# Optimization experiments

Measured on AMD Instinct MI355X. Metric: run time of the kernel, lower is better.

## Reference

```python
import jax, jax.numpy as jnp
import numpy as np

N = 50000
DIM_IN = 256
HID = 64
OUT = 32
E1 = 800000
E2 = 1600000
BN_EPS = 1e-5


def _make_edges(rng, n, e):
    row = rng.integers(0, n, size=e).astype(np.int32)
    col = rng.integers(0, n, size=e).astype(np.int32)
    # gcn_norm without self loops: val = d^{-1/2}[row] * d^{-1/2}[col]
    deg = np.bincount(row, minlength=n) + 0.0
    deg_c = np.bincount(col, minlength=n) + 0.0
    dr = 1.0 / np.sqrt(np.maximum(deg, 1.0))
    dc = 1.0 / np.sqrt(np.maximum(deg_c, 1.0))
    val = (dr[row] * dc[col]).astype(np.float32)
    return row, col, val


def setup_inputs() -> dict:
    key = jax.random.key(0)
    ks = jax.random.split(key, 4)
    rng = np.random.default_rng(0)
    e1_row, e1_col, e1_val = _make_edges(rng, N, E1)
    e2_row, e2_col, e2_val = _make_edges(rng, N, E2)
    return {
        "x": jax.random.normal(ks[0], (N, DIM_IN), dtype=jnp.float32),
        "e1_row": jnp.asarray(e1_row), "e1_col": jnp.asarray(e1_col), "e1_val": jnp.asarray(e1_val),
        "e2_row": jnp.asarray(e2_row), "e2_col": jnp.asarray(e2_col), "e2_val": jnp.asarray(e2_val),
        "W_embed": jax.random.normal(ks[1], (DIM_IN, HID), dtype=jnp.float32) * (1.0 / np.sqrt(DIM_IN)),
        "b_embed": jnp.zeros((HID,), dtype=jnp.float32),
        "bn0_gamma": jnp.ones((2 * HID,), dtype=jnp.float32),
        "bn0_beta": jnp.zeros((2 * HID,), dtype=jnp.float32),
        "bn1_gamma": jnp.ones((4 * HID,), dtype=jnp.float32),
        "bn1_beta": jnp.zeros((4 * HID,), dtype=jnp.float32),
        "W_head": jax.random.normal(ks[2], (15 * HID, OUT), dtype=jnp.float32) * (1.0 / np.sqrt(15 * HID)),
        "b_head": jnp.zeros((OUT,), dtype=jnp.float32),
    }


def _spmm(row, col, val, x, n):
    # out[row] += val * x[col]  (sparse [n,n] @ dense [n,d])
    return jax.ops.segment_sum(val[:, None] * x[col], row, num_segments=n)


def _bn(v, gamma, beta):
    # BatchNorm1d training-mode math: per-feature mean / biased var over nodes
    m = jnp.mean(v, axis=0)
    var = jnp.mean(jnp.square(v - m), axis=0)
    return gamma * (v - m) * jax.lax.rsqrt(var + BN_EPS) + beta


def reference(x, e1_row, e1_col, e1_val, e2_row, e2_col, e2_val,
              W_embed, b_embed, bn0_gamma, bn0_beta, bn1_gamma, bn1_beta,
              W_head, b_head):
    n = x.shape[0]

    def conv(h):
        h1 = _spmm(e1_row, e1_col, e1_val, h, n)
        h2 = _spmm(e2_row, e2_col, e2_val, h, n)
        return jnp.concatenate([h1, h2], axis=1)

    h = jax.nn.relu(x @ W_embed + b_embed)          # [n, HID]
    xs = [h]
    c0 = _bn(conv(h), bn0_gamma, bn0_beta)           # [n, 2*HID]
    xs.append(c0)
    c1 = _bn(conv(c0), bn1_gamma, bn1_beta)          # [n, 4*HID]
    xs.append(c1)
    c2 = conv(c1)                                    # [n, 8*HID]
    xs.append(c2)
    j = jnp.concatenate(xs, axis=1)                  # [n, 15*HID]
    return j @ W_head + b_head                       # [n, OUT]
```

## Files before the change

### kernel.cpp

```cpp
#include <hip/hip_runtime.h>


#define NN  50000
#define E1N 800000
#define E2N 1600000
#define LD  960
#define NT  3125
#define NBKT 391
#define CHUNK 2048
#define G1B 391
#define G2B 782
#define NCG 7

typedef short bf16x8 __attribute__((ext_vector_type(8)));
typedef float f32x4  __attribute__((ext_vector_type(4)));
typedef float f32x2  __attribute__((ext_vector_type(2)));

__device__ __forceinline__ float bfl(unsigned int w) { return __uint_as_float(w << 16); }
__device__ __forceinline__ float bfh(unsigned int w) { return __uint_as_float(w & 0xFFFF0000u); }
__device__ __forceinline__ float bf2f(unsigned short u) { return __uint_as_float(((unsigned int)u) << 16); }
__device__ __forceinline__ unsigned short f2bf(float f) {
    unsigned int u = __float_as_uint(f);
    u += 0x7FFFu + ((u >> 16) & 1u);
    return (unsigned short)(u >> 16);
}
__device__ __forceinline__ unsigned int pack2(float a, float b) {
    return (unsigned int)f2bf(a) | ((unsigned int)f2bf(b) << 16);
}
__device__ __forceinline__ unsigned int packfp8(float a, float b, float c, float d) {
    int w = __builtin_amdgcn_cvt_pk_fp8_f32(a, b, 0, false);
    w     = __builtin_amdgcn_cvt_pk_fp8_f32(c, d, w, true);
    return (unsigned int)w;
}
__device__ __forceinline__ f32x2 pkfma(f32x2 a, f32x2 b, f32x2 c) {
#if __has_builtin(__builtin_elementwise_fma)
    return __builtin_elementwise_fma(a, b, c);
#else
    return (f32x2){fmaf(a[0], b[0], c[0]), fmaf(a[1], b[1], c[1])};
#endif
}
__device__ __forceinline__ f32x2 bf2(unsigned int w) {
    return (f32x2){bfl(w), bfh(w)};
}


__global__ __launch_bounds__(256) void zero_kernel(float* c, int nc) {
    int i = blockIdx.x * 256 + threadIdx.x;
    if (i < nc) c[i] = 0.f;
}

__global__ __launch_bounds__(256) void bucket_count_kernel(const int* __restrict__ r1,
                                                           const int* __restrict__ r2,
                                                           int* __restrict__ bc1, int* __restrict__ bc2) {
    __shared__ int cnt[NBKT];
    for (int t = threadIdx.x; t < NBKT; t += 256) cnt[t] = 0;
    __syncthreads();
    int blk = blockIdx.x;
    const int* r; int base, lim; int* bc;
    if (blk < G1B) { r = r1; base = blk * CHUNK; lim = min(base + CHUNK, E1N); bc = bc1 + blk * NBKT; }
    else { int b2 = blk - G1B; r = r2; base = b2 * CHUNK; lim = min(base + CHUNK, E2N); bc = bc2 + b2 * NBKT; }
    for (int i = base + threadIdx.x; i < lim; i += 256)
        atomicAdd(&cnt[r[i] >> 7], 1);
    __syncthreads();
    for (int t = threadIdx.x; t < NBKT; t += 256) bc[t] = cnt[t];
}

__global__ __launch_bounds__(512) void bucket_scan_kernel(int* __restrict__ bc1, int* __restrict__ bc2) {
    __shared__ int s[512];
    int t = threadIdx.x;
    int tot1 = 0, tot2 = 0;
    if (t < NBKT) {
        for (int b = 0; b < G1B; b++) tot1 += bc1[b * NBKT + t];
        for (int b = 0; b < G2B; b++) tot2 += bc2[b * NBKT + t];
    }
    s[t] = (t < NBKT) ? tot1 : 0;
    __syncthreads();
    for (int off = 1; off < 512; off <<= 1) {
        int v = (t >= off) ? s[t - off] : 0;
        __syncthreads(); s[t] += v; __syncthreads();
    }
    int base1 = ((t < NBKT) ? s[t] : 0) - tot1;
    __syncthreads();
    s[t] = (t < NBKT) ? tot2 : 0;
    __syncthreads();
    for (int off = 1; off < 512; off <<= 1) {
        int v = (t >= off) ? s[t - off] : 0;
        __syncthreads(); s[t] += v; __syncthreads();
    }
    int base2 = ((t < NBKT) ? s[t] : 0) - tot2;
    if (t < NBKT) {
        int run = base1;
        for (int b = 0; b < G1B; b++) { int v = bc1[b * NBKT + t]; bc1[b * NBKT + t] = run; run += v; }
        run = base2;
        for (int b = 0; b < G2B; b++) { int v = bc2[b * NBKT + t]; bc2[b * NBKT + t] = run; run += v; }
    }
}

__global__ __launch_bounds__(256) void bucket_place_kernel(
        const int* __restrict__ r1, const int* __restrict__ c1, const float* __restrict__ v1,
        const int* __restrict__ r2, const int* __restrict__ c2, const float* __restrict__ v2,
        const int* __restrict__ bc1, const int* __restrict__ bc2,
        uint2* __restrict__ T1, uint2* __restrict__ T2) {
    __shared__ int pos[NBKT];
    int blk = blockIdx.x;
    const int *r, *c; const float* v; int base, lim; const int* bc; uint2* T;
    if (blk < G1B) { r = r1; c = c1; v = v1; base = blk * CHUNK; lim = min(base + CHUNK, E1N);
                     bc = bc1 + blk * NBKT; T = T1; }
    else { int b2 = blk - G1B; r = r2; c = c2; v = v2; base = b2 * CHUNK; lim = min(base + CHUNK, E2N);
           bc = bc2 + b2 * NBKT; T = T2; }
    for (int t = threadIdx.x; t < NBKT; t += 256) pos[t] = bc[t];
    __syncthreads();
    for (int i = base + threadIdx.x; i < lim; i += 256) {
        int row = r[i];
        int p = atomicAdd(&pos[row >> 7], 1);
        T[p] = make_uint2(((unsigned)c[i] << 16) | (unsigned)row, __float_as_uint(v[i]));
    }
}

__global__ __launch_bounds__(256) void bucket_sort_kernel(
        const int* __restrict__ bb1, const uint2* __restrict__ T1, int* __restrict__ rp1, unsigned int* __restrict__ Ed1,
        const int* __restrict__ bb2, const uint2* __restrict__ T2, int* __restrict__ rp2, unsigned int* __restrict__ Ed2) {
    int b = blockIdx.x % NBKT;
    int g = blockIdx.x / NBKT;
    const int* bb = g ? bb2 : bb1;
    const uint2* T = g ? T2 : T1;
    int* rp = g ? rp2 : rp1;
    unsigned int* Ed = g ? Ed2 : Ed1;
    int EN = g ? E2N : E1N;
    int beg = bb[b];
    int end = (b == NBKT - 1) ? EN : bb[b + 1];
    int R0 = b * 128;
    int nrows = min(128, NN - R0);
    __shared__ int cnt[1024];
    __shared__ int cur[896];
    __shared__ int ps[256];
    int t = threadIdx.x;
    for (int i = t; i < 1024; i += 256) cnt[i] = 0;
    __syncthreads();
    for (int i = beg + t; i < end; i += 256) {
        unsigned int x = T[i].x;
        int lr = (x & 0xFFFFu) & 127;
        int cg = (int)(x >> 29);
        atomicAdd(&cnt[lr * NCG + cg + 1], 1);
    }
    __syncthreads();
    int b0 = t * 4;
    int c0 = cnt[b0], c1 = cnt[b0 + 1], c2 = cnt[b0 + 2], c3 = cnt[b0 + 3];
    int s1 = c0 + c1, s2 = s1 + c2, s3 = s2 + c3;
    ps[t] = s3;
    __syncthreads();
    for (int off = 1; off < 256; off <<= 1) {
        int v = (t >= off) ? ps[t - off] : 0;
        __syncthreads(); ps[t] += v; __syncthreads();
    }
    int base = (t > 0) ? ps[t - 1] : 0;
    cnt[b0] = base + c0; cnt[b0 + 1] = base + s1;
    cnt[b0 + 2] = base + s2; cnt[b0 + 3] = base + s3;
    __syncthreads();
    for (int k = t; k < 896; k += 256) cur[k] = beg + cnt[k];
    if (t < nrows) rp[R0 + t] = beg + cnt[t * NCG];
    if (b == NBKT - 1 && t == 0) rp[NN] = end;
    __syncthreads();
    for (int i = beg + t; i < end; i += 256) {
        uint2 rec = T[i];
        int lr = (rec.x & 0xFFFFu) & 127;
        int cg = (int)(rec.x >> 29);
        int p = atomicAdd(&cur[lr * NCG + cg], 1);
        Ed[p] = (rec.x & 0xFFFF0000u) | (unsigned)f2bf(__uint_as_float(rec.y));
    }
}

__global__ __launch_bounds__(256) void packw_kernel(const float* __restrict__ W, unsigned short* __restrict__ Wb,
                                                    int NC, int kbs, int total) {
    int i = blockIdx.x * 256 + threadIdx.x;
    if (i >= total) return;
    int lane  = i & 63;
    int kb    = (i >> 6) % kbs;
    int ctile = i / (kbs * 64);
    int n  = ctile * 16 + (lane & 15);
    int k0 = kb * 32 + (lane >> 4) * 8;
    unsigned short v[8];
    #pragma unroll
    for (int j = 0; j < 8; j++) v[j] = f2bf(W[(k0 + j) * NC + n]);
    *(uint4*)(Wb + (size_t)i * 8) = *(uint4*)v;
}

__global__ __launch_bounds__(256) void embed_mfma_kernel(const float* __restrict__ x,
                                                         const unsigned short* __restrict__ Wb,
                                                         const float* __restrict__ bias,
                                                         unsigned short* __restrict__ Jh) {
    int wave = threadIdx.x >> 6;
    int lane = threadIdx.x & 63;
    int tile = blockIdx.x * 4 + wave;
    if (tile >= NT) return;
    int m = lane & 15;
    int q = lane >> 4;
    const float* xr = x + (size_t)(tile * 16 + m) * 256 + q * 8;
    const unsigned short* bbase = Wb + (size_t)lane * 8;
    f32x4 acc[4];
    #pragma unroll
    for (int ct = 0; ct < 4; ct++) acc[ct] = (f32x4){0.f, 0.f, 0.f, 0.f};
    #pragma unroll
    for (int kb = 0; kb < 8; kb++) {
        float4 xa = *(const float4*)(xr + kb * 32);
        float4 xb = *(const float4*)(xr + kb * 32 + 4);
        unsigned short av[8];
        av[0] = f2bf(xa.x); av[1] = f2bf(xa.y); av[2] = f2bf(xa.z); av[3] = f2bf(xa.w);
        av[4] = f2bf(xb.x); av[5] = f2bf(xb.y); av[6] = f2bf(xb.z); av[7] = f2bf(xb.w);
        bf16x8 a = *(bf16x8*)av;
        #pragma unroll
        for (int ct = 0; ct < 4; ct++) {
            bf16x8 bfr = *(const bf16x8*)(bbase + (size_t)(ct * 8 + kb) * 512);
            acc[ct] = __builtin_amdgcn_mfma_f32_16x16x32_bf16(a, bfr, acc[ct], 0, 0, 0);
        }
    }
    #pragma unroll
    for (int ct = 0; ct < 4; ct++) {
        int col = ct * 16 + m;
        float bb = bias[col];
        #pragma unroll
        for (int r = 0; r < 4; r++) {
            float v = fmaxf(acc[ct][r] + bb, 0.f);
            Jh[(size_t)(tile * 16 + q * 4 + r) * LD + col] = f2bf(v);
        }
    }
}

template <int LPR>
__global__ __launch_bounds__(256) void spmm_bf16x8_kernel(
        const int* __restrict__ rp1, const unsigned int* __restrict__ ed1,
        const int* __restrict__ rp2, const unsigned int* __restrict__ ed2,
        const unsigned short* __restrict__ src, unsigned short* __restrict__ dst) {
    constexpr int ROWS = 64 / LPR;
    constexpr int SRCF = LPR * 8;
    constexpr int RPB  = ROWS * 4;
    constexpr int GB   = (NN + RPB - 1) / RPB;
    int g    = (blockIdx.x >= GB) ? 1 : 0;
    int bx   = blockIdx.x - g * GB;
    int wave = threadIdx.x >> 6;
    int lane = threadIdx.x & 63;
    int grp  = lane / LPR;
    int sub  = lane % LPR;
    int row  = (bx * 4 + wave) * ROWS + grp;
    const int*          rp = g ? rp2 : rp1;
    const unsigned int* ed = g ? ed2 : ed1;
    bool ok = row < NN;
    int beg = 0, end = 0;
    if (ok) { beg = rp[row]; end = rp[row + 1]; }

    f32x2 acc[4];
    #pragma unroll
    for (int u = 0; u < 4; u++) acc[u] = (f32x2){0.f, 0.f};
    const unsigned short* sbase = src + sub * 8;

    int j = beg;
    for (; j + 8 <= end; j += 8) {
        unsigned int e[8];
        #pragma unroll
        for (int u = 0; u < 8; u++) e[u] = ed[j + u];
        uint4 s[8];
        #pragma unroll
        for (int u = 0; u < 8; u++) s[u] = *(const uint4*)(sbase + (size_t)(e[u] >> 16) * LD);
        #pragma unroll
        for (int u = 0; u < 8; u++) {
            float v = bfl(e[u]);
            f32x2 vv = (f32x2){v, v};
            acc[0] = pkfma(vv, bf2(s[u].x), acc[0]);
            acc[1] = pkfma(vv, bf2(s[u].y), acc[1]);
            acc[2] = pkfma(vv, bf2(s[u].z), acc[2]);
            acc[3] = pkfma(vv, bf2(s[u].w), acc[3]);
        }
    }
    for (; j < end; j++) {
        unsigned int e = ed[j];
        float v = bfl(e);
        f32x2 vv = (f32x2){v, v};
        uint4 s = *(const uint4*)(sbase + (size_t)(e >> 16) * LD);
        acc[0] = pkfma(vv, bf2(s.x), acc[0]);
        acc[1] = pkfma(vv, bf2(s.y), acc[1]);
        acc[2] = pkfma(vv, bf2(s.z), acc[2]);
        acc[3] = pkfma(vv, bf2(s.w), acc[3]);
    }

    if (ok) {
        unsigned short* dp = dst + (size_t)row * LD + g * SRCF + sub * 8;
        uint4 o;
        o.x = pack2(acc[0][0], acc[0][1]); o.y = pack2(acc[1][0], acc[1][1]);
        o.z = pack2(acc[2][0], acc[2][1]); o.w = pack2(acc[3][0], acc[3][1]);
        *(uint4*)dp = o;
    }
}

template <int LPR>
__global__ __launch_bounds__(256) void spmm_fp8x16_kernel(
        const int* __restrict__ rp1, const unsigned int* __restrict__ ed1,
        const int* __restrict__ rp2, const unsigned int* __restrict__ ed2,
        const unsigned char* __restrict__ src8,
        unsigned short* __restrict__ dst) {
    constexpr int ROWS = 64 / LPR;
    constexpr int SRCF = LPR * 16;
    constexpr int RPB  = ROWS * 4;
    constexpr int GB   = (NN + RPB - 1) / RPB;
    int g    = (blockIdx.x >= GB) ? 1 : 0;
    int bx   = blockIdx.x - g * GB;
    int wave = threadIdx.x >> 6;
    int lane = threadIdx.x & 63;
    int grp  = lane / LPR;
    int sub  = lane % LPR;
    int row  = (bx * 4 + wave) * ROWS + grp;
    const int*          rp = g ? rp2 : rp1;
    const unsigned int* ed = g ? ed2 : ed1;
    bool ok = row < NN;
    int beg = 0, end = 0;
    if (ok) { beg = rp[row]; end = rp[row + 1]; }

    f32x2 acc[8];
    #pragma unroll
    for (int u = 0; u < 8; u++) acc[u] = (f32x2){0.f, 0.f};
    const unsigned char* sbase = src8 + sub * 16;

    int j = beg;
    for (; j + 8 <= end; j += 8) {
        unsigned int e[8];
        #pragma unroll
        for (int u = 0; u < 8; u++) e[u] = ed[j + u];
        uint4 s[8];
        #pragma unroll
        for (int u = 0; u < 8; u++) s[u] = *(const uint4*)(sbase + (size_t)(e[u] >> 16) * SRCF);
        #pragma unroll
        for (int u = 0; u < 8; u++) {
            float v = bfl(e[u]);
            f32x2 vv = (f32x2){v, v};
            acc[0] = pkfma(vv, __builtin_amdgcn_cvt_pk_f32_fp8(s[u].x, false), acc[0]);
            acc[1] = pkfma(vv, __builtin_amdgcn_cvt_pk_f32_fp8(s[u].x, true),  acc[1]);
            acc[2] = pkfma(vv, __builtin_amdgcn_cvt_pk_f32_fp8(s[u].y, false), acc[2]);
            acc[3] = pkfma(vv, __builtin_amdgcn_cvt_pk_f32_fp8(s[u].y, true),  acc[3]);
            acc[4] = pkfma(vv, __builtin_amdgcn_cvt_pk_f32_fp8(s[u].z, false), acc[4]);
            acc[5] = pkfma(vv, __builtin_amdgcn_cvt_pk_f32_fp8(s[u].z, true),  acc[5]);
            acc[6] = pkfma(vv, __builtin_amdgcn_cvt_pk_f32_fp8(s[u].w, false), acc[6]);
            acc[7] = pkfma(vv, __builtin_amdgcn_cvt_pk_f32_fp8(s[u].w, true),  acc[7]);
        }
    }
    for (; j < end; j++) {
        unsigned int e = ed[j];
        float v = bfl(e);
        f32x2 vv = (f32x2){v, v};
        uint4 s = *(const uint4*)(sbase + (size_t)(e >> 16) * SRCF);
        acc[0] = pkfma(vv, __builtin_amdgcn_cvt_pk_f32_fp8(s.x, false), acc[0]);
        acc[1] = pkfma(vv, __builtin_amdgcn_cvt_pk_f32_fp8(s.x, true),  acc[1]);
        acc[2] = pkfma(vv, __builtin_amdgcn_cvt_pk_f32_fp8(s.y, false), acc[2]);
        acc[3] = pkfma(vv, __builtin_amdgcn_cvt_pk_f32_fp8(s.y, true),  acc[3]);
        acc[4] = pkfma(vv, __builtin_amdgcn_cvt_pk_f32_fp8(s.z, false), acc[4]);
        acc[5] = pkfma(vv, __builtin_amdgcn_cvt_pk_f32_fp8(s.z, true),  acc[5]);
        acc[6] = pkfma(vv, __builtin_amdgcn_cvt_pk_f32_fp8(s.w, false), acc[6]);
        acc[7] = pkfma(vv, __builtin_amdgcn_cvt_pk_f32_fp8(s.w, true),  acc[7]);
    }

    if (ok) {
        unsigned short* dp = dst + (size_t)row * LD + g * SRCF + sub * 16;
        uint4 o1, o2;
        o1.x = pack2(acc[0][0], acc[0][1]); o1.y = pack2(acc[1][0], acc[1][1]);
        o1.z = pack2(acc[2][0], acc[2][1]); o1.w = pack2(acc[3][0], acc[3][1]);
        o2.x = pack2(acc[4][0], acc[4][1]); o2.y = pack2(acc[5][0], acc[5][1]);
        o2.z = pack2(acc[6][0], acc[6][1]); o2.w = pack2(acc[7][0], acc[7][1]);
        *(uint4*)dp = o1;
        *(uint4*)(dp + 8) = o2;
    }
}

template <int F>
__global__ __launch_bounds__(256) void bn_stats_kernel(const unsigned short* __restrict__ c,
                                                       float* sum, float* sumsq) {
    constexpr int SL = 256 / F;
    int f  = threadIdx.x % F;
    int sl = threadIdx.x / F;
    float s = 0.f, ss = 0.f;
    for (int r = blockIdx.x * SL + sl; r < NN; r += gridDim.x * SL) {
        float v = bf2f(c[(size_t)r * LD + f]);
        s += v; ss += v * v;
    }
    __shared__ float ls[256], lss[256];
    ls[threadIdx.x] = s; lss[threadIdx.x] = ss;
    __syncthreads();
    if (sl == 0) {
        #pragma unroll
        for (int u = 1; u < SL; u++) { s += ls[f + u * F]; ss += lss[f + u * F]; }
        atomicAdd(&sum[f], s);
        atomicAdd(&sumsq[f], ss);
    }
}

__global__ void bn_finalize_kernel(const float* sum, const float* sumsq, const float* __restrict__ gamma,
                                   const float* __restrict__ beta, float* scale, float* shift, int F) {
    int f = blockIdx.x * blockDim.x + threadIdx.x;
    if (f >= F) return;
    float m   = sum[f] * (1.0f / NN);
    float var = sumsq[f] * (1.0f / NN) - m * m;
    float sc  = gamma[f] * rsqrtf(var + 1e-5f);
    scale[f] = sc;
    shift[f] = beta[f] - m * sc;
}

template <int F>
__global__ __launch_bounds__(256) void bn_apply_kernel(unsigned short* __restrict__ c,
                                                       const float* __restrict__ scale,
                                                       const float* __restrict__ shift) {
    constexpr int FV = F / 4;
    int idx  = blockIdx.x * 256 + threadIdx.x;
    int node = idx / FV;
    int fo   = (idx % FV) * 4;
    if (node >= NN) return;
    unsigned short* p = c + (size_t)node * LD + fo;
    uint2 v = *(uint2*)p;
    float a0 = bfl(v.x), a1 = bfh(v.x), a2 = bfl(v.y), a3 = bfh(v.y);
    float4 sc = *(const float4*)(scale + fo);
    float4 sh = *(const float4*)(shift + fo);
    a0 = fmaf(a0, sc.x, sh.x);
    a1 = fmaf(a1, sc.y, sh.y);
    a2 = fmaf(a2, sc.z, sh.z);
    a3 = fmaf(a3, sc.w, sh.w);
    v.x = pack2(a0, a1); v.y = pack2(a2, a3);
    *(uint2*)p = v;
}

__global__ __launch_bounds__(256) void bn_apply_fp8_kernel(unsigned short* __restrict__ c,
                                                           unsigned char* __restrict__ c8,
                                                           const float* __restrict__ scale,
                                                           const float* __restrict__ shift) {
    int idx  = blockIdx.x * 256 + threadIdx.x;
    int node = idx >> 6;
    int fo   = (idx & 63) * 4;
    if (node >= NN) return;
    unsigned short* p = c + (size_t)node * LD + fo;
    uint2 v = *(uint2*)p;
    float a0 = bfl(v.x), a1 = bfh(v.x), a2 = bfl(v.y), a3 = bfh(v.y);
    float4 sc = *(const float4*)(scale + fo);
    float4 sh = *(const float4*)(shift + fo);
    a0 = fmaf(a0, sc.x, sh.x);
    a1 = fmaf(a1, sc.y, sh.y);
    a2 = fmaf(a2, sc.z, sh.z);
    a3 = fmaf(a3, sc.w, sh.w);
    v.x = pack2(a0, a1); v.y = pack2(a2, a3);
    *(uint2*)p = v;
    *(unsigned int*)(c8 + (size_t)node * 256 + fo) = packfp8(a0, a1, a2, a3);
}

__global__ __launch_bounds__(256) void head_mfma_kernel(const unsigned short* __restrict__ Jh,
                                                        const unsigned short* __restrict__ Wb,
                                                        const float* __restrict__ b,
                                                        float* __restrict__ out) {
    int wave = threadIdx.x >> 6;
    int lane = threadIdx.x & 63;
    int tile = blockIdx.x * 4 + wave;
    if (tile >= NT) return;
    int m = lane & 15;
    int q = lane >> 4;
    const unsigned short* arow  = Jh + (size_t)(tile * 16 + m) * LD + q * 8;
    const unsigned short* bbase = Wb + (size_t)lane * 8;
    f32x4 acc0 = {0.f, 0.f, 0.f, 0.f};
    f32x4 acc1 = {0.f, 0.f, 0.f, 0.f};
    #pragma unroll 5
    for (int kb = 0; kb < 30; kb++) {
        bf16x8 a  = *(const bf16x8*)(arow + kb * 32);
        bf16x8 b0 = *(const bf16x8*)(bbase + (size_t)kb * 512);
        bf16x8 b1 = *(const bf16x8*)(bbase + (size_t)(30 + kb) * 512);
        acc0 = __builtin_amdgcn_mfma_f32_16x16x32_bf16(a, b0, acc0, 0, 0, 0);
        acc1 = __builtin_amdgcn_mfma_f32_16x16x32_bf16(a, b1, acc1, 0, 0, 0);
    }
    int col = m;
    float b0 = b[col], b1 = b[16 + col];
    #pragma unroll
    for (int r = 0; r < 4; r++) {
        float* op = out + (size_t)(tile * 16 + q * 4 + r) * 32 + col;
        op[0]  = acc0[r] + b0;
        op[16] = acc1[r] + b1;
    }
}


extern "C" void kernel_launch(void* const* d_in, const int* in_sizes, int n_in,
                              void* d_out, int out_size, void* d_ws, size_t ws_size,
                              hipStream_t stream) {
    const float* x      = (const float*)d_in[0];
    const int*   e1_row = (const int*)d_in[1];
    const int*   e1_col = (const int*)d_in[2];
    const float* e1_val = (const float*)d_in[3];
    const int*   e2_row = (const int*)d_in[4];
    const int*   e2_col = (const int*)d_in[5];
    const float* e2_val = (const float*)d_in[6];
    const float* W_emb  = (const float*)d_in[7];
    const float* b_emb  = (const float*)d_in[8];
    const float* bn0_g  = (const float*)d_in[9];
    const float* bn0_b  = (const float*)d_in[10];
    const float* bn1_g  = (const float*)d_in[11];
    const float* bn1_b  = (const float*)d_in[12];
    const float* W_head = (const float*)d_in[13];
    const float* b_head = (const float*)d_in[14];
    float* out = (float*)d_out;

    char* ws = (char*)d_ws;
    auto alloc = [&](size_t bytes) -> char* {
        char* p = ws;
        ws += (bytes + 255) & ~(size_t)255;
        return p;
    };
    int*   rp1   = (int*)alloc((NN + 1) * 4);
    int*   rp2   = (int*)alloc((NN + 1) * 4);
    int*   bc1   = (int*)alloc((size_t)G1B * NBKT * 4);
    int*   bc2   = (int*)alloc((size_t)G2B * NBKT * 4);
    unsigned int* Ed1 = (unsigned int*)alloc((size_t)E1N * 4);
    unsigned int* Ed2 = (unsigned int*)alloc((size_t)E2N * 4);
    float* stats = (float*)alloc(1536 * 4);
    unsigned short* Wbh  = (unsigned short*)alloc(3840 * 8 * 2);
    unsigned short* Wbe  = (unsigned short*)alloc(2048 * 8 * 2);
    unsigned char*  C1f8 = (unsigned char*)alloc((size_t)NN * 256);
    unsigned short* Jh   = (unsigned short*)alloc((size_t)NN * LD * 2);
    uint2* T1 = (uint2*)Jh;
    uint2* T2 = T1 + E1N;

    float* sum0   = stats;        float* sq0    = stats + 128;
    float* sum1   = stats + 256;  float* sq1    = stats + 512;
    float* scale0 = stats + 768;  float* shift0 = stats + 896;
    float* scale1 = stats + 1024; float* shift1 = stats + 1280;

    zero_kernel<<<3, 256, 0, stream>>>(stats, 768);
    bucket_count_kernel<<<G1B + G2B, 256, 0, stream>>>(e1_row, e2_row, bc1, bc2);
    bucket_scan_kernel<<<1, 512, 0, stream>>>(bc1, bc2);
    bucket_place_kernel<<<G1B + G2B, 256, 0, stream>>>(e1_row, e1_col, e1_val,
                                                       e2_row, e2_col, e2_val, bc1, bc2, T1, T2);
    bucket_sort_kernel<<<2 * NBKT, 256, 0, stream>>>(bc1, T1, rp1, Ed1, bc2, T2, rp2, Ed2);
    packw_kernel<<<15, 256, 0, stream>>>(W_head, Wbh, 32, 30, 3840);
    packw_kernel<<<8, 256, 0, stream>>>(W_emb, Wbe, 64, 8, 2048);

    embed_mfma_kernel<<<(NT + 3) / 4, 256, 0, stream>>>(x, Wbe, b_emb, Jh);

    spmm_bf16x8_kernel<8><<<2 * ((NN + 31) / 32), 256, 0, stream>>>(rp1, Ed1, rp2, Ed2, Jh, Jh + 64);
    bn_stats_kernel<128><<<512, 256, 0, stream>>>(Jh + 64, sum0, sq0);
    bn_finalize_kernel<<<1, 128, 0, stream>>>(sum0, sq0, bn0_g, bn0_b, scale0, shift0, 128);
    bn_apply_kernel<128><<<(NN * 32 + 255) / 256, 256, 0, stream>>>(Jh + 64, scale0, shift0);

    spmm_bf16x8_kernel<16><<<2 * (NN / 16), 256, 0, stream>>>(rp1, Ed1, rp2, Ed2, Jh + 64, Jh + 192);
    bn_stats_kernel<256><<<512, 256, 0, stream>>>(Jh + 192, sum1, sq1);
    bn_finalize_kernel<<<1, 256, 0, stream>>>(sum1, sq1, bn1_g, bn1_b, scale1, shift1, 256);
    bn_apply_fp8_kernel<<<(NN * 64 + 255) / 256, 256, 0, stream>>>(Jh + 192, C1f8, scale1, shift1);

    spmm_fp8x16_kernel<16><<<2 * (NN / 16), 256, 0, stream>>>(rp1, Ed1, rp2, Ed2, C1f8, Jh + 448);

    head_mfma_kernel<<<(NT + 3) / 4, 256, 0, stream>>>(Jh, Wbh, b_head, out);
}
```

Baseline: 632.6 us.

## Parallelize bucket offset scan across many blocks instead of single block

Replaces the single-block bucket scan, where each of 391 threads serially walked up to 782 chunk counts twice, with three kernels: a per-bucket reduction over 782 blocks, a small single-block exclusive scan of bucket totals, and a per-bucket parallel scan that writes chunk offsets. The aim is to remove a long serial, latency-bound pass from the preprocessing. It adds two extra kernel launches and a small workspace for totals and bases. scan_apply assumes at most 1024 chunks per graph, which holds for G2B=782.

```diff
diff --git a/kernel.cpp b/kernel.cpp
--- a/kernel.cpp
+++ b/kernel.cpp
@@ -65,34 +65,75 @@
     for (int t = threadIdx.x; t < NBKT; t += 256) bc[t] = cnt[t];
 }
 
-__global__ __launch_bounds__(512) void bucket_scan_kernel(int* __restrict__ bc1, int* __restrict__ bc2) {
+__global__ __launch_bounds__(256) void scan_tot_kernel(const int* __restrict__ bc1,
+                                                       const int* __restrict__ bc2,
+                                                       int* __restrict__ tot) {
+    int b = blockIdx.x % NBKT;
+    int g = blockIdx.x / NBKT;
+    const int* bc = g ? bc2 : bc1;
+    int G = g ? G2B : G1B;
+    int s = 0;
+    for (int i = threadIdx.x; i < G; i += 256) s += bc[(size_t)i * NBKT + b];
+    __shared__ int red[256];
+    red[threadIdx.x] = s;
+    __syncthreads();
+    for (int off = 128; off; off >>= 1) {
+        if ((int)threadIdx.x < off) red[threadIdx.x] += red[threadIdx.x + off];
+        __syncthreads();
+    }
+    if (threadIdx.x == 0) tot[g * NBKT + b] = red[0];
+}
+
+__global__ __launch_bounds__(512) void scan_base_kernel(const int* __restrict__ tot,
+                                                        int* __restrict__ base) {
     __shared__ int s[512];
     int t = threadIdx.x;
-    int tot1 = 0, tot2 = 0;
-    if (t < NBKT) {
-        for (int b = 0; b < G1B; b++) tot1 += bc1[b * NBKT + t];
-        for (int b = 0; b < G2B; b++) tot2 += bc2[b * NBKT + t];
-    }
-    s[t] = (t < NBKT) ? tot1 : 0;
+    int v1 = (t < NBKT) ? tot[t] : 0;
+    s[t] = v1;
     __syncthreads();
     for (int off = 1; off < 512; off <<= 1) {
         int v = (t >= off) ? s[t - off] : 0;
         __syncthreads(); s[t] += v; __syncthreads();
     }
-    int base1 = ((t < NBKT) ? s[t] : 0) - tot1;
-    __syncthreads();
-    s[t] = (t < NBKT) ? tot2 : 0;
+    if (t < NBKT) base[t] = s[t] - v1;
+    __syncthreads();
+    int v2 = (t < NBKT) ? tot[NBKT + t] : 0;
+    s[t] = v2;
     __syncthreads();
     for (int off = 1; off < 512; off <<= 1) {
         int v = (t >= off) ? s[t - off] : 0;
         __syncthreads(); s[t] += v; __syncthreads();
     }
-    int base2 = ((t < NBKT) ? s[t] : 0) - tot2;
-    if (t < NBKT) {
-        int run = base1;
-        for (int b = 0; b < G1B; b++) { int v = bc1[b * NBKT + t]; bc1[b * NBKT + t] = run; run += v; }
-        run = base2;
-        for (int b = 0; b < G2B; b++) { int v = bc2[b * NBKT + t]; bc2[b * NBKT + t] = run; run += v; }
+    if (t < NBKT) base[NBKT + t] = s[t] - v2;
+}
+
+__global__ __launch_bounds__(256) void scan_apply_kernel(int* __restrict__ bc1, int* __restrict__ bc2,
+                                                         const int* __restrict__ base) {
+    int b = blockIdx.x % NBKT;
+    int g = blockIdx.x / NBKT;
+    int* bc = g ? bc2 : bc1;
+    int G = g ? G2B : G1B;
+    int t = threadIdx.x;
+    int vals[4];
+    int loc = 0;
+    #pragma unroll
+    for (int k = 0; k < 4; k++) {
+        int idx = t * 4 + k;
+        int v = (idx < G) ? bc[(size_t)idx * NBKT + b] : 0;
+        vals[k] = v; loc += v;
+    }
+    __shared__ int s[256];
+    s[t] = loc;
+    __syncthreads();
+    for (int off = 1; off < 256; off <<= 1) {
+        int v = (t >= off) ? s[t - off] : 0;
+        __syncthreads(); s[t] += v; __syncthreads();
+    }
+    int run = base[g * NBKT + b] + ((t > 0) ? s[t - 1] : 0);
+    #pragma unroll
+    for (int k = 0; k < 4; k++) {
+        int idx = t * 4 + k;
+        if (idx < G) { int old = vals[k]; bc[(size_t)idx * NBKT + b] = run; run += old; }
     }
 }
 
@@ -508,6 +549,8 @@
     int*   rp2   = (int*)alloc((NN + 1) * 4);
     int*   bc1   = (int*)alloc((size_t)G1B * NBKT * 4);
     int*   bc2   = (int*)alloc((size_t)G2B * NBKT * 4);
+    int*   tot   = (int*)alloc(2 * NBKT * 4);
+    int*   basep = (int*)alloc(2 * NBKT * 4);
     unsigned int* Ed1 = (unsigned int*)alloc((size_t)E1N * 4);
     unsigned int* Ed2 = (unsigned int*)alloc((size_t)E2N * 4);
     float* stats = (float*)alloc(1536 * 4);
@@ -525,7 +568,9 @@
 
     zero_kernel<<<3, 256, 0, stream>>>(stats, 768);
     bucket_count_kernel<<<G1B + G2B, 256, 0, stream>>>(e1_row, e2_row, bc1, bc2);
-    bucket_scan_kernel<<<1, 512, 0, stream>>>(bc1, bc2);
+    scan_tot_kernel<<<2 * NBKT, 256, 0, stream>>>(bc1, bc2, tot);
+    scan_base_kernel<<<1, 512, 0, stream>>>(tot, basep);
+    scan_apply_kernel<<<2 * NBKT, 256, 0, stream>>>(bc1, bc2, basep);
     bucket_place_kernel<<<G1B + G2B, 256, 0, stream>>>(e1_row, e1_col, e1_val,
                                                        e2_row, e2_col, e2_val, bc1, bc2, T1, T2);
     bucket_sort_kernel<<<2 * NBKT, 256, 0, stream>>>(bc1, T1, rp1, Ed1, bc2, T2, rp2, Ed2);
```

After: 528.0 us (median of 2 runs). 1.2x faster.
